# Kernel optimization log

Hardware: AMD Instinct MI355X
Metric: run time of the kernel (lower is better)

Reference implementation:

```python
import jax, jax.numpy as jnp
import numpy as np

BN_EPS = 1e-5


def setup_inputs() -> dict:
    key = jax.random.key(0)
    ks = jax.random.split(key, 9)
    B, C, H, W = 2, 64, 128, 128
    Ci = 32  # inter_channels
    sc = 0.05
    x = jax.random.normal(ks[0], (B, C, H, W), jnp.float32)
    g_w = jax.random.normal(ks[1], (Ci, C), jnp.float32) * sc
    g_b = jax.random.normal(ks[2], (Ci,), jnp.float32) * sc
    theta_w = jax.random.normal(ks[3], (Ci, C), jnp.float32) * sc
    theta_b = jax.random.normal(ks[4], (Ci,), jnp.float32) * sc
    phi_w = jax.random.normal(ks[5], (Ci, C), jnp.float32) * sc
    phi_b = jax.random.normal(ks[6], (Ci,), jnp.float32) * sc
    w_w = jax.random.normal(ks[7], (C, Ci), jnp.float32) * sc
    w_b = jnp.zeros((C,), jnp.float32)
    # BatchNorm affine params (random so the block is non-trivial; the torch
    # code zero-inits them, which would make the whole block an identity).
    bn_gamma = 1.0 + 0.1 * jax.random.normal(ks[8], (C,), jnp.float32)
    bn_beta = jnp.zeros((C,), jnp.float32)
    return dict(x=x, g_w=g_w, g_b=g_b, theta_w=theta_w, theta_b=theta_b,
                phi_w=phi_w, phi_b=phi_b, w_w=w_w, w_b=w_b,
                bn_gamma=bn_gamma, bn_beta=bn_beta)


def reference(x, g_w, g_b, theta_w, theta_b, phi_w, phi_b, w_w, w_b,
              bn_gamma, bn_beta):
    B, C, H, W = x.shape
    Ci = g_w.shape[0]
    H1, W1 = H // 2, W // 2

    def block(xq):  # embedded-gaussian non-local block on one quadrant group [B,C,h,w]
        b, c, h, w = xq.shape
        n = h * w
        xf = xq.reshape(b, c, n)                                  # [B,C,N]
        th = jnp.einsum('oc,bcn->bno', theta_w, xf) + theta_b     # [B,N,Ci]
        ph = jnp.einsum('oc,bcn->bon', phi_w, xf) + phi_b[:, None]  # [B,Ci,N]
        gx = jnp.einsum('oc,bcn->bno', g_w, xf) + g_b             # [B,N,Ci]
        f = jnp.einsum('bno,bom->bnm', th, ph)                    # [B,N,N] affinity
        a = jax.nn.softmax(f, axis=-1)
        y = jnp.einsum('bnm,bmo->bno', a, gx)                     # [B,N,Ci]
        wy = jnp.einsum('co,bno->bcn', w_w, y) + w_b[:, None]     # [B,C,N]
        wy = wy.reshape(b, c, h, w)
        # BatchNorm2d, training-mode batch stats (per quadrant call in torch)
        mu = wy.mean(axis=(0, 2, 3), keepdims=True)
        var = wy.var(axis=(0, 2, 3), keepdims=True)
        bn = (wy - mu) * jax.lax.rsqrt(var + BN_EPS)
        bn = bn * bn_gamma[None, :, None, None] + bn_beta[None, :, None, None]
        return bn + xq                                            # residual

    # split into 4 quadrants: [B,C,H,W] -> [4,B,C,H1,W1] (quadrant-major)
    xq = x.reshape(B, C, 2, H1, 2, W1).transpose(2, 4, 0, 1, 3, 5)
    xq = xq.reshape(4, B, C, H1, W1)
    zq = jax.vmap(block)(xq)                                      # [4,B,C,H1,W1]
    # reassemble
    z = zq.reshape(2, 2, B, C, H1, W1).transpose(2, 3, 0, 4, 1, 5)
    return z.reshape(B, C, H, W)
```

## Files before the change

kernel.cpp:

```cpp
#include <hip/hip_runtime.h>
#include <stdint.h>

typedef __bf16 bf16x8 __attribute__((ext_vector_type(8)));
typedef short  short4v __attribute__((ext_vector_type(4)));
typedef float  floatx4 __attribute__((ext_vector_type(4)));
typedef uint32_t u32x4 __attribute__((ext_vector_type(4)));

#define DI __device__ __forceinline__

DI uint16_t bf1(float a) {
    union { __bf16 h; uint16_t u; } r; r.h = (__bf16)a; return r.u;
}

__global__ __launch_bounds__(512) void proj_kernel(
    const float* __restrict__ x,
    const float* __restrict__ tw, const float* __restrict__ tb,
    const float* __restrict__ pw, const float* __restrict__ pb,
    const float* __restrict__ gw, const float* __restrict__ gb,
    uint16_t* __restrict__ th, uint16_t* __restrict__ phT,
    uint16_t* __restrict__ vP)
{
    __shared__ uint16_t ldsg[32 * 68];
    int blk = blockIdx.x & 7, nt = blockIdx.x >> 3;
    int tid = threadIdx.x, wid = tid >> 6, lane = tid & 63;
    int quad = lane >> 4, low = lane & 15;
    int pwv = wid & 3, oh = wid >> 2;

    int b = blk & 1, q = blk >> 1, qh = q >> 1, qw = q & 1;
    int pixA = pwv * 16 + low;
    const float* xg = x + (size_t)b * 1048576 +
                      (size_t)(qh * 64 + nt) * 128 + qw * 64 + pixA;

    float a0[8], a1[8];
#pragma unroll
    for (int j = 0; j < 8; ++j) {
        a0[j] = xg[(size_t)(quad * 8 + j) * 16384];
        a1[j] = xg[(size_t)(32 + quad * 8 + j) * 16384];
    }
    bf16x8 A0, A1;
#pragma unroll
    for (int j = 0; j < 8; ++j) {
        A0[j] = (__bf16)a0[j];
        A1[j] = (__bf16)a1[j];
    }

    int o = oh * 16 + low;
    auto dotile = [&](const float* W, const float* Bv) -> floatx4 {
        floatx4 acc;
        float bias = Bv[o];
#pragma unroll
        for (int r = 0; r < 4; ++r) acc[r] = bias;
        const float* wr = W + o * 64 + quad * 8;
        floatx4 w0a = *(const floatx4*)(wr);
        floatx4 w0b = *(const floatx4*)(wr + 4);
        floatx4 w1a = *(const floatx4*)(wr + 32);
        floatx4 w1b = *(const floatx4*)(wr + 36);
        bf16x8 B0, B1;
#pragma unroll
        for (int j = 0; j < 4; ++j) {
            B0[j]     = (__bf16)w0a[j];
            B0[j + 4] = (__bf16)w0b[j];
            B1[j]     = (__bf16)w1a[j];
            B1[j + 4] = (__bf16)w1b[j];
        }
        acc = __builtin_amdgcn_mfma_f32_16x16x32_bf16(A0, B0, acc, 0, 0, 0);
        acc = __builtin_amdgcn_mfma_f32_16x16x32_bf16(A1, B1, acc, 0, 0, 0);
        return acc;
    };

    size_t thbase = ((size_t)blk * 4096 + nt * 64 + pwv * 16 + quad * 4) * 32;

    floatx4 t0 = dotile(tw, tb);
#pragma unroll
    for (int r = 0; r < 4; ++r)
        th[thbase + r * 32 + o] = bf1(t0[r] * 1.44269504088896f);
    floatx4 p0 = dotile(pw, pb);
#pragma unroll
    for (int r = 0; r < 4; ++r)
        phT[thbase + r * 32 + o] = bf1(p0[r]);
    floatx4 g0 = dotile(gw, gb);
#pragma unroll
    for (int r = 0; r < 4; ++r)
        ldsg[o * 68 + pwv * 16 + quad * 4 + r] = bf1(g0[r]);
    __syncthreads();
    if (tid < 256) {
        int oo = tid >> 3, k = (tid & 7) * 8;
        const uint16_t* src = &ldsg[oo * 68 + k];
        uint64_t lo = *(const uint64_t*)(src);
        uint64_t hi = *(const uint64_t*)(src + 4);
        union { uint64_t q2[2]; u32x4 v; } out;
        out.q2[0] = lo; out.q2[1] = hi;
        *(u32x4*)(vP + (size_t)blk * 131072 + nt * 2048 + tid * 8) = out.v;
    }
}

__global__ __launch_bounds__(512, 4) void flash_kernel(
    const uint16_t* __restrict__ th, const uint16_t* __restrict__ phT,
    const uint16_t* __restrict__ vP, const float* __restrict__ w_w,
    const float* __restrict__ w_b, float* __restrict__ wy,
    float2* __restrict__ partials)
{
    __shared__ uint16_t ldsK[4][2][64 * 40];
    __shared__ uint16_t ldsV[4][2][32 * 72];
    __shared__ float sred[2][64][2];
    int blk = blockIdx.x & 7;
    int rg  = blockIdx.x >> 3;
    int tid = threadIdx.x, wid = tid >> 6, lane = tid & 63;
    int sp = wid >> 1, qg = wid & 1;
    int lt = tid & 127;
    int quad = lane >> 4, low = lane & 15;
    int n0 = rg * 64 + qg * 32;

    const uint16_t* thB = th  + (size_t)blk * 131072;
    const uint16_t* kG  = phT + (size_t)blk * 131072;
    const uint16_t* vG  = vP  + (size_t)blk * 131072;

    bf16x8 qfA = *(const bf16x8*)(thB + (n0 + low) * 32 + quad * 8);
    bf16x8 qfB = *(const bf16x8*)(thB + (n0 + 16 + low) * 32 + quad * 8);

    const u32x4* kSrc = (const u32x4*)kG + sp * 4096 + lt;
    const u32x4* vSrc = (const u32x4*)vG + sp * 4096 + lt;
    const int kW0 = ((lt >> 2)) * 40 + (lt & 3) * 8;
    const int kW1 = (32 + (lt >> 2)) * 40 + (lt & 3) * 8;
    const int vW0 = ((lt >> 3)) * 72 + (lt & 7) * 8;
    const int vW1 = (16 + (lt >> 3)) * 72 + (lt & 7) * 8;

    u32x4 kr0 = kSrc[0], kr1 = kSrc[128];
    u32x4 vr0 = vSrc[0], vr1 = vSrc[128];
    *(u32x4*)(&ldsK[sp][0][kW0]) = kr0;  *(u32x4*)(&ldsK[sp][0][kW1]) = kr1;
    *(u32x4*)(&ldsV[sp][0][vW0]) = vr0;  *(u32x4*)(&ldsV[sp][0][vW1]) = vr1;
    __syncthreads();

    floatx4 zero = {0.f, 0.f, 0.f, 0.f};
    floatx4 oaA0 = zero, oaA1 = zero, osA = zero;
    floatx4 oaB0 = zero, oaB1 = zero, osB = zero;
    union { uint32_t u[4]; bf16x8 v; } ones8;
    ones8.u[0] = 0x3F803F80u; ones8.u[1] = 0x3F803F80u;
    ones8.u[2] = 0x3F803F80u; ones8.u[3] = 0x3F803F80u;

    for (int t = 0; t < 16; ++t) {
        int buf = t & 1;
        if (t < 15) {
            kr0 = kSrc[(t + 1) * 256];  kr1 = kSrc[(t + 1) * 256 + 128];
            vr0 = vSrc[(t + 1) * 256];  vr1 = vSrc[(t + 1) * 256 + 128];
        }
        const uint16_t* Kb = ldsK[sp][buf];
        const uint16_t* Vb = ldsV[sp][buf];
        bf16x8 kf[4];
        union { short4v s[2]; bf16x8 v; } vA2[2], vB2[2];
#pragma unroll
        for (int c = 0; c < 4; ++c)
            kf[c] = *(const bf16x8*)(Kb + (c * 16 + low) * 40 + quad * 8);
#pragma unroll
        for (int c2 = 0; c2 < 2; ++c2) {
            vA2[c2].s[0] = *(const short4v*)(Vb + low * 72 + (2*c2)     * 16 + quad * 4);
            vA2[c2].s[1] = *(const short4v*)(Vb + low * 72 + (2*c2 + 1) * 16 + quad * 4);
            vB2[c2].s[0] = *(const short4v*)(Vb + (16 + low) * 72 + (2*c2)     * 16 + quad * 4);
            vB2[c2].s[1] = *(const short4v*)(Vb + (16 + low) * 72 + (2*c2 + 1) * 16 + quad * 4);
        }
        {
            floatx4 sa[4];
#pragma unroll
            for (int c = 0; c < 4; ++c)
                sa[c] = __builtin_amdgcn_mfma_f32_16x16x32_bf16(kf[c], qfA, zero, 0, 0, 0);
            union { __bf16 h[8]; bf16x8 v; } P2[2];
#pragma unroll
            for (int c2 = 0; c2 < 2; ++c2) {
#pragma unroll
                for (int j = 0; j < 4; ++j) {
                    P2[c2].h[j]     = (__bf16)__builtin_amdgcn_exp2f(sa[2*c2][j]);
                    P2[c2].h[4 + j] = (__bf16)__builtin_amdgcn_exp2f(sa[2*c2 + 1][j]);
                }
            }
#pragma unroll
            for (int c2 = 0; c2 < 2; ++c2) {
                oaA0 = __builtin_amdgcn_mfma_f32_16x16x32_bf16(vA2[c2].v, P2[c2].v, oaA0, 0, 0, 0);
                oaA1 = __builtin_amdgcn_mfma_f32_16x16x32_bf16(vB2[c2].v, P2[c2].v, oaA1, 0, 0, 0);
                osA  = __builtin_amdgcn_mfma_f32_16x16x32_bf16(ones8.v,   P2[c2].v, osA,  0, 0, 0);
            }
        }
        {
            floatx4 sa[4];
#pragma unroll
            for (int c = 0; c < 4; ++c)
                sa[c] = __builtin_amdgcn_mfma_f32_16x16x32_bf16(kf[c], qfB, zero, 0, 0, 0);
            union { __bf16 h[8]; bf16x8 v; } P2[2];
#pragma unroll
            for (int c2 = 0; c2 < 2; ++c2) {
#pragma unroll
                for (int j = 0; j < 4; ++j) {
                    P2[c2].h[j]     = (__bf16)__builtin_amdgcn_exp2f(sa[2*c2][j]);
                    P2[c2].h[4 + j] = (__bf16)__builtin_amdgcn_exp2f(sa[2*c2 + 1][j]);
                }
            }
#pragma unroll
            for (int c2 = 0; c2 < 2; ++c2) {
                oaB0 = __builtin_amdgcn_mfma_f32_16x16x32_bf16(vA2[c2].v, P2[c2].v, oaB0, 0, 0, 0);
                oaB1 = __builtin_amdgcn_mfma_f32_16x16x32_bf16(vB2[c2].v, P2[c2].v, oaB1, 0, 0, 0);
                osB  = __builtin_amdgcn_mfma_f32_16x16x32_bf16(ones8.v,   P2[c2].v, osB,  0, 0, 0);
            }
        }
        if (t < 15) {
            *(u32x4*)(&ldsK[sp][buf ^ 1][kW0]) = kr0;
            *(u32x4*)(&ldsK[sp][buf ^ 1][kW1]) = kr1;
            *(u32x4*)(&ldsV[sp][buf ^ 1][vW0]) = vr0;
            *(u32x4*)(&ldsV[sp][buf ^ 1][vW1]) = vr1;
        }
        __syncthreads();
    }

    {
        float* exW = (float*)(&ldsK[0][0][0]);
        int li = tid * 18;
#pragma unroll
        for (int r = 0; r < 4; ++r) {
            exW[li + r]      = oaA0[r];
            exW[li + 4 + r]  = oaA1[r];
            exW[li + 9 + r]  = oaB0[r];
            exW[li + 13 + r] = oaB1[r];
        }
        exW[li + 8]  = osA[0];
        exW[li + 17] = osB[0];
    }
    __syncthreads();
    floatx4 cA0 = zero, cA1 = zero, cB0 = zero, cB1 = zero;
    float cosA = 0.f, cosB = 0.f;
    {
        const float* exR = (const float*)(&ldsK[0][0][0]);
#pragma unroll
        for (int s = 0; s < 4; ++s) {
            const float* p = exR + (s * 128 + lt) * 18;
#pragma unroll
            for (int r = 0; r < 4; ++r) {
                cA0[r] += p[r];
                cA1[r] += p[4 + r];
                cB0[r] += p[9 + r];
                cB1[r] += p[13 + r];
            }
            cosA += p[8];
            cosB += p[17];
        }
    }

    float rinvA = 1.0f / cosA, rinvB = 1.0f / cosB;
    union { __bf16 h[8]; bf16x8 v; } YA8, YB8;
#pragma unroll
    for (int r = 0; r < 4; ++r) {
        YA8.h[r]     = (__bf16)(cA0[r] * rinvA);
        YA8.h[4 + r] = (__bf16)(cA1[r] * rinvA);
        YB8.h[r]     = (__bf16)(cB0[r] * rinvB);
        YB8.h[4 + r] = (__bf16)(cB1[r] * rinvB);
    }

    float* wyB = wy + (size_t)blk * 262144;
    int nA = n0 + low, nB = n0 + 16 + low;
    int ct = sp;
    {
        floatx4 accA, accB;
#pragma unroll
        for (int r = 0; r < 4; ++r) {
            accA[r] = w_b[ct * 16 + quad * 4 + r];
            accB[r] = accA[r];
        }
        floatx4 w0 = *(const floatx4*)(w_w + (ct * 16 + low) * 32 + quad * 4);
        floatx4 w1 = *(const floatx4*)(w_w + (ct * 16 + low) * 32 + 16 + quad * 4);
        union { __bf16 h[8]; bf16x8 v; } W8;
#pragma unroll
        for (int r = 0; r < 4; ++r) {
            W8.h[r]     = (__bf16)w0[r];
            W8.h[4 + r] = (__bf16)w1[r];
        }
        accA = __builtin_amdgcn_mfma_f32_16x16x32_bf16(W8.v, YA8.v, accA, 0, 0, 0);
        accB = __builtin_amdgcn_mfma_f32_16x16x32_bf16(W8.v, YB8.v, accB, 0, 0, 0);
#pragma unroll
        for (int r = 0; r < 4; ++r) {
            int ch = ct * 16 + quad * 4 + r;
            wyB[(size_t)ch * 4096 + nA] = accA[r];
            wyB[(size_t)ch * 4096 + nB] = accB[r];
            float s = accA[r] + accB[r];
            float ss = accA[r] * accA[r] + accB[r] * accB[r];
            s += __shfl_xor(s, 1); ss += __shfl_xor(ss, 1);
            s += __shfl_xor(s, 2); ss += __shfl_xor(ss, 2);
            s += __shfl_xor(s, 4); ss += __shfl_xor(ss, 4);
            s += __shfl_xor(s, 8); ss += __shfl_xor(ss, 8);
            if (low == 0) {
                sred[qg][ch][0] = s;
                sred[qg][ch][1] = ss;
            }
        }
    }
    __syncthreads();
    if (tid < 64) {
        float s  = sred[0][tid][0] + sred[1][tid][0];
        float ss = sred[0][tid][1] + sred[1][tid][1];
        partials[((size_t)blk * 64 + rg) * 64 + tid] = make_float2(s, ss);
    }
}

__global__ __launch_bounds__(64) void stats_kernel(
    const float2* __restrict__ partials, const float* __restrict__ gamma,
    const float* __restrict__ beta, float2* __restrict__ stats)
{
    int q = blockIdx.x >> 6, c = blockIdx.x & 63;
    int t = threadIdx.x;
    float2 p0 = partials[(((size_t)(q * 2 + 0)) * 64 + t) * 64 + c];
    float2 p1 = partials[(((size_t)(q * 2 + 1)) * 64 + t) * 64 + c];
    float S = p0.x + p1.x, SS = p0.y + p1.y;
    S += __shfl_xor(S, 1);  SS += __shfl_xor(SS, 1);
    S += __shfl_xor(S, 2);  SS += __shfl_xor(SS, 2);
    S += __shfl_xor(S, 4);  SS += __shfl_xor(SS, 4);
    S += __shfl_xor(S, 8);  SS += __shfl_xor(SS, 8);
    S += __shfl_xor(S, 16); SS += __shfl_xor(SS, 16);
    S += __shfl_xor(S, 32); SS += __shfl_xor(SS, 32);
    if (t == 0) {
        float mu  = S * (1.0f / 8192.0f);
        float var = SS * (1.0f / 8192.0f) - mu * mu;
        float scale = gamma[c] * rsqrtf(var + 1e-5f);
        float shift = beta[c] - mu * scale;
        stats[q * 64 + c] = make_float2(scale, shift);
    }
}

__global__ __launch_bounds__(256) void final_kernel(
    const float* __restrict__ wy, const float2* __restrict__ stats,
    const float* __restrict__ x, float* __restrict__ out)
{
    int bid = blockIdx.x;
    size_t base = (((size_t)(bid & 7) * 256 + (bid >> 3)) * 256 + threadIdx.x) * 4;
    int n   = (int)(base & 4095);
    int c   = (int)((base >> 12) & 63);
    int blk = (int)(base >> 18);
    int b = blk & 1, q = blk >> 1, qh = q >> 1, qw = q & 1;
    int i = n >> 6, j = n & 63;
    float2 sc = stats[q * 64 + c];
    floatx4 wv = *(const floatx4*)(wy + base);
    size_t xa = ((size_t)(b * 64 + c) * 128 + (qh * 64 + i)) * 128 + qw * 64 + j;
    floatx4 xv = *(const floatx4*)(x + xa);
    floatx4 ov;
#pragma unroll
    for (int k = 0; k < 4; ++k) ov[k] = wv[k] * sc.x + sc.y + xv[k];
    *(floatx4*)(out + xa) = ov;
}

extern "C" void kernel_launch(void* const* d_in, const int* in_sizes, int n_in,
                              void* d_out, int out_size, void* d_ws, size_t ws_size,
                              hipStream_t stream)
{
    const float* x       = (const float*)d_in[0];
    const float* g_w     = (const float*)d_in[1];
    const float* g_b     = (const float*)d_in[2];
    const float* theta_w = (const float*)d_in[3];
    const float* theta_b = (const float*)d_in[4];
    const float* phi_w   = (const float*)d_in[5];
    const float* phi_b   = (const float*)d_in[6];
    const float* w_w     = (const float*)d_in[7];
    const float* w_b     = (const float*)d_in[8];
    const float* gamma   = (const float*)d_in[9];
    const float* beta    = (const float*)d_in[10];

    char* ws = (char*)d_ws;
    uint16_t* th       = (uint16_t*)(ws);
    uint16_t* phT      = (uint16_t*)(ws + (2u << 20));
    uint16_t* vP       = (uint16_t*)(ws + (4u << 20));
    float*    wy       = (float*)(ws + (6u << 20));
    float2*   partials = (float2*)(ws + (14u << 20));
    float2*   stats    = (float2*)(ws + (14u << 20) + (1u << 18));

    proj_kernel  <<<512,  512, 0, stream>>>(x, theta_w, theta_b, phi_w, phi_b,
                                            g_w, g_b, th, phT, vP);
    flash_kernel <<<512,  512, 0, stream>>>(th, phT, vP, w_w, w_b, wy, partials);
    stats_kernel <<<256,  64,  0, stream>>>(partials, gamma, beta, stats);
    final_kernel <<<2048, 256, 0, stream>>>(wy, stats, x, (float*)d_out);
}
```

Baseline: 123.6 us.

## Fuse BN stats reduction into final kernel and add MFMA priority hints

Removes the separate stats kernel launch: each final-kernel block now reduces the 128 partial sums for its quadrant/channel, computes the BN scale and shift in shared memory, and applies them. This saves one launch and its dependency gap, at the cost of redundant partial-sum reads and two block barriers in every final block. It also wraps the MFMA groups in the flash kernel with s_setprio to raise wave priority during matrix work, hoping to interleave better with exp and LDS work from other waves.

```diff
diff --git a/kernel.cpp b/kernel.cpp
--- a/kernel.cpp
+++ b/kernel.cpp
@@ -160,9 +160,11 @@
         }
         {
             floatx4 sa[4];
+            __builtin_amdgcn_s_setprio(1);
 #pragma unroll
             for (int c = 0; c < 4; ++c)
                 sa[c] = __builtin_amdgcn_mfma_f32_16x16x32_bf16(kf[c], qfA, zero, 0, 0, 0);
+            __builtin_amdgcn_s_setprio(0);
             union { __bf16 h[8]; bf16x8 v; } P2[2];
 #pragma unroll
             for (int c2 = 0; c2 < 2; ++c2) {
@@ -172,18 +174,22 @@
                     P2[c2].h[4 + j] = (__bf16)__builtin_amdgcn_exp2f(sa[2*c2 + 1][j]);
                 }
             }
+            __builtin_amdgcn_s_setprio(1);
 #pragma unroll
             for (int c2 = 0; c2 < 2; ++c2) {
                 oaA0 = __builtin_amdgcn_mfma_f32_16x16x32_bf16(vA2[c2].v, P2[c2].v, oaA0, 0, 0, 0);
                 oaA1 = __builtin_amdgcn_mfma_f32_16x16x32_bf16(vB2[c2].v, P2[c2].v, oaA1, 0, 0, 0);
                 osA  = __builtin_amdgcn_mfma_f32_16x16x32_bf16(ones8.v,   P2[c2].v, osA,  0, 0, 0);
             }
+            __builtin_amdgcn_s_setprio(0);
         }
         {
             floatx4 sa[4];
+            __builtin_amdgcn_s_setprio(1);
 #pragma unroll
             for (int c = 0; c < 4; ++c)
                 sa[c] = __builtin_amdgcn_mfma_f32_16x16x32_bf16(kf[c], qfB, zero, 0, 0, 0);
+            __builtin_amdgcn_s_setprio(0);
             union { __bf16 h[8]; bf16x8 v; } P2[2];
 #pragma unroll
             for (int c2 = 0; c2 < 2; ++c2) {
@@ -193,12 +199,14 @@
                     P2[c2].h[4 + j] = (__bf16)__builtin_amdgcn_exp2f(sa[2*c2 + 1][j]);
                 }
             }
+            __builtin_amdgcn_s_setprio(1);
 #pragma unroll
             for (int c2 = 0; c2 < 2; ++c2) {
                 oaB0 = __builtin_amdgcn_mfma_f32_16x16x32_bf16(vA2[c2].v, P2[c2].v, oaB0, 0, 0, 0);
                 oaB1 = __builtin_amdgcn_mfma_f32_16x16x32_bf16(vB2[c2].v, P2[c2].v, oaB1, 0, 0, 0);
                 osB  = __builtin_amdgcn_mfma_f32_16x16x32_bf16(ones8.v,   P2[c2].v, osB,  0, 0, 0);
             }
+            __builtin_amdgcn_s_setprio(0);
         }
         if (t < 15) {
             *(u32x4*)(&ldsK[sp][buf ^ 1][kW0]) = kr0;
@@ -297,42 +305,50 @@
     }
 }
 
-__global__ __launch_bounds__(64) void stats_kernel(
-    const float2* __restrict__ partials, const float* __restrict__ gamma,
-    const float* __restrict__ beta, float2* __restrict__ stats)
+__global__ __launch_bounds__(256) void final_kernel(
+    const float* __restrict__ wy, const float2* __restrict__ partials,
+    const float* __restrict__ gamma, const float* __restrict__ beta,
+    const float* __restrict__ x, float* __restrict__ out)
 {
-    int q = blockIdx.x >> 6, c = blockIdx.x & 63;
-    int t = threadIdx.x;
-    float2 p0 = partials[(((size_t)(q * 2 + 0)) * 64 + t) * 64 + c];
-    float2 p1 = partials[(((size_t)(q * 2 + 1)) * 64 + t) * 64 + c];
-    float S = p0.x + p1.x, SS = p0.y + p1.y;
+    __shared__ float2 ssh[2];
+    __shared__ float2 scsh;
+    int bid = blockIdx.x;
+    int tid = threadIdx.x;
+    int qq = (bid & 7) >> 1;
+    int cc = (bid >> 5) & 63;
+
+    float S = 0.f, SS = 0.f;
+    if (tid < 128) {
+        int b = tid >> 6, rg = tid & 63;
+        float2 p = partials[(((size_t)(qq * 2 + b)) * 64 + rg) * 64 + cc];
+        S = p.x; SS = p.y;
+    }
     S += __shfl_xor(S, 1);  SS += __shfl_xor(SS, 1);
     S += __shfl_xor(S, 2);  SS += __shfl_xor(SS, 2);
     S += __shfl_xor(S, 4);  SS += __shfl_xor(SS, 4);
     S += __shfl_xor(S, 8);  SS += __shfl_xor(SS, 8);
     S += __shfl_xor(S, 16); SS += __shfl_xor(SS, 16);
     S += __shfl_xor(S, 32); SS += __shfl_xor(SS, 32);
-    if (t == 0) {
-        float mu  = S * (1.0f / 8192.0f);
-        float var = SS * (1.0f / 8192.0f) - mu * mu;
-        float scale = gamma[c] * rsqrtf(var + 1e-5f);
-        float shift = beta[c] - mu * scale;
-        stats[q * 64 + c] = make_float2(scale, shift);
-    }
-}
-
-__global__ __launch_bounds__(256) void final_kernel(
-    const float* __restrict__ wy, const float2* __restrict__ stats,
-    const float* __restrict__ x, float* __restrict__ out)
-{
-    int bid = blockIdx.x;
-    size_t base = (((size_t)(bid & 7) * 256 + (bid >> 3)) * 256 + threadIdx.x) * 4;
+    if (tid < 128 && (tid & 63) == 0) ssh[tid >> 6] = make_float2(S, SS);
+    __syncthreads();
+    if (tid == 0) {
+        float St  = ssh[0].x + ssh[1].x;
+        float SSt = ssh[0].y + ssh[1].y;
+        float mu  = St * (1.0f / 8192.0f);
+        float var = SSt * (1.0f / 8192.0f) - mu * mu;
+        float scale = gamma[cc] * rsqrtf(var + 1e-5f);
+        float shift = beta[cc] - mu * scale;
+        scsh = make_float2(scale, shift);
+    }
+    __syncthreads();
+    float2 sc = scsh;
+
+    size_t base = (((size_t)(bid & 7) * 256 + (bid >> 3)) * 256 + tid) * 4;
     int n   = (int)(base & 4095);
     int c   = (int)((base >> 12) & 63);
     int blk = (int)(base >> 18);
     int b = blk & 1, q = blk >> 1, qh = q >> 1, qw = q & 1;
     int i = n >> 6, j = n & 63;
-    float2 sc = stats[q * 64 + c];
     floatx4 wv = *(const floatx4*)(wy + base);
     size_t xa = ((size_t)(b * 64 + c) * 128 + (qh * 64 + i)) * 128 + qw * 64 + j;
     floatx4 xv = *(const floatx4*)(x + xa);
@@ -364,11 +380,10 @@
     uint16_t* vP       = (uint16_t*)(ws + (4u << 20));
     float*    wy       = (float*)(ws + (6u << 20));
     float2*   partials = (float2*)(ws + (14u << 20));
-    float2*   stats    = (float2*)(ws + (14u << 20) + (1u << 18));
 
     proj_kernel  <<<512,  512, 0, stream>>>(x, theta_w, theta_b, phi_w, phi_b,
                                             g_w, g_b, th, phT, vP);
     flash_kernel <<<512,  512, 0, stream>>>(th, phT, vP, w_w, w_b, wy, partials);
-    stats_kernel <<<256,  64,  0, stream>>>(partials, gamma, beta, stats);
-    final_kernel <<<2048, 256, 0, stream>>>(wy, stats, x, (float*)d_out);
-}
+    final_kernel <<<2048, 256, 0, stream>>>(wy, partials, gamma, beta, x,
+                                            (float*)d_out);
+}
```

After: 123.3 us. Within noise of the previous version (-0.2%).
